# Kernel optimization log

Measured on AMD Instinct MI355X. Metric: run time of the kernel, lower is better.

Reference implementation:

```python
import jax, jax.numpy as jnp
import numpy as np

B, T, C, H, W = 8, 8, 32, 16, 28
NH, DK = 4, 8                 # n_head, d_k == d_v
RADIUS = [3, 3, 3, 3]
DILATION = [1, 3, 5, 7]
LN_EPS = 1e-5


def setup_inputs() -> dict:
    key = jax.random.key(0)
    ks = jax.random.split(key, 8)
    s = 1.0 / np.sqrt(C).astype(np.float32)
    return {
        "first": jax.random.normal(ks[0], (B, T, C, H, W), jnp.float32),
        "x": jax.random.normal(ks[1], (B, T, C, H, W), jnp.float32),
        "Wq": jax.random.normal(ks[2], (NH * DK, C), jnp.float32) * s,
        "Wk": jax.random.normal(ks[3], (NH * DK, C), jnp.float32) * s,
        "Wv": jax.random.normal(ks[4], (NH * DK, C), jnp.float32) * s,
        "Wo": jax.random.normal(ks[5], (C, NH * DK), jnp.float32) * s,
        "ln_gamma": 1.0 + 0.1 * jax.random.normal(ks[6], (DK, H, W), jnp.float32),
        "ln_beta": 0.1 * jax.random.normal(ks[7], (DK, H, W), jnp.float32),
    }


def _shift(x, dy, dx):
    # out[..., i, j] = x[..., i+dy, j+dx]; zero out-of-bounds. mask: (H, W) valid.
    h, w = x.shape[-2:]
    xs = jnp.roll(x, (-dy, -dx), axis=(-2, -1))
    mh = (jnp.arange(h) + dy >= 0) & (jnp.arange(h) + dy < h)
    mw = (jnp.arange(w) + dx >= 0) & (jnp.arange(w) + dx < w)
    m = mh[:, None] & mw[None, :]
    return jnp.where(m, xs, 0.0), m


def _head_attn(q, k, v, radius, dilation, scale):
    # q,k,v: (b,t,c,h,w). Returns softmaxed scores P (b,t,O*t,h,w) and
    # aggregation T (b,t,c,h,w). Aggregation uses RAW scaled scores (as the repo
    # does: spatial_temporal_aggregation receives M_A_i, not its softmax).
    b, t, c, h, w = q.shape
    scores, vals, masks = [], [], []
    for dy in range(-radius, radius + 1):
        for dx in range(-radius, radius + 1):
            ks, m = _shift(k, dy * dilation, dx * dilation)
            vs, _ = _shift(v, dy * dilation, dx * dilation)
            # score against all source frames s at the shifted spatial location
            scores.append(jnp.einsum('btchw,bschw->btshw', q, ks))
            vals.append(vs)
            masks.append(m)
    A = jnp.stack(scores, axis=2)                      # (b,t,O,s,h,w), O=(2r+1)^2
    M = jnp.stack(masks, axis=0)                       # (O,h,w)
    A = jnp.where(M[None, None, :, None], A / scale, -jnp.inf)
    O = A.shape[2]
    P = jax.nn.softmax(A.reshape(b, t, O * t, h, w), axis=2)
    Wm = jnp.where(M[None, None, :, None], A, 0.0)     # skip invalid (-inf) slots
    V = jnp.stack(vals, axis=0)                        # (O,b,s,c,h,w)
    Tout = jnp.einsum('btoshw,obschw->btchw', Wm, V)
    return P, Tout


def reference(first, x, Wq, Wk, Wv, Wo, ln_gamma, ln_beta):
    b, t, c, h, w = x.shape
    q = jnp.einsum('btchw,oc->btohw', first, Wq).reshape(b, t, NH, DK, h, w)
    k = jnp.einsum('btchw,oc->btohw', x, Wk).reshape(b, t, NH, DK, h, w)
    v = jnp.einsum('btchw,oc->btohw', x, Wv).reshape(b, t, NH, DK, h, w)
    scale = float(np.sqrt(C / NH))
    Ps, Ts = [], []
    for i in range(NH):
        qi = q[:, :, i]
        mu = jnp.mean(qi, axis=(2, 3, 4), keepdims=True)
        var = jnp.var(qi, axis=(2, 3, 4), keepdims=True)
        qi = (qi - mu) / jnp.sqrt(var + LN_EPS) * ln_gamma + ln_beta
        P, Ti = _head_attn(qi, k[:, :, i], v[:, :, i], RADIUS[i], DILATION[i], scale)
        Ps.append(P)
        Ts.append(Ti)
    M_S = jnp.max(jnp.concatenate(Ps, axis=2), axis=2)   # (b,t,h,w)
    M_T = jnp.concatenate(Ts, axis=2)                    # (b,t,NH*DK,h,w)
    out = jnp.einsum('btchw,oc->btohw', M_T, Wo) * M_S[:, :, None]
    return out
```

## Files before the change

kernel.cpp:

```cpp
#include <hip/hip_runtime.h>

#define Bc 8
#define Tc 8
#define Cc 32
#define Hc 16
#define Wc 28
#define NHc 4
#define DKc 8
#define HWc (Hc*Wc)
#define INV_SCALE 0.35355339059327373f
#define LN_EPSc 1e-5f

typedef _Float16 half8 __attribute__((ext_vector_type(8)));


__global__ __launch_bounds__(448) void qkv_ln_kernel(
    const float* __restrict__ first, const float* __restrict__ x,
    const float* __restrict__ Wq, const float* __restrict__ Wk,
    const float* __restrict__ Wv,
    const float* __restrict__ gamma, const float* __restrict__ beta,
    float4* __restrict__ Q, float* __restrict__ K, float* __restrict__ V)
{
    int blk  = blockIdx.x;
    int head = blk % NHc;
    int bt   = blk / NHc;
    int t    = bt % Tc;
    int b    = bt / Tc;
    int tid  = threadIdx.x;

    const float* fp = first + (size_t)bt * Cc * HWc + tid;
    const float* xp = x     + (size_t)bt * Cc * HWc + tid;
    float fv[Cc], xv[Cc];
#pragma unroll
    for (int c = 0; c < Cc; ++c) { fv[c] = fp[c*HWc]; xv[c] = xp[c*HWc]; }

    float qv[DKc], kv[DKc], vv[DKc];
#pragma unroll
    for (int dk = 0; dk < DKc; ++dk) {
        int o = head*DKc + dk;
        float aq = 0.f, ak = 0.f, av = 0.f;
#pragma unroll
        for (int c = 0; c < Cc; ++c) {
            aq = fmaf(Wq[o*Cc+c], fv[c], aq);
            ak = fmaf(Wk[o*Cc+c], xv[c], ak);
            av = fmaf(Wv[o*Cc+c], xv[c], av);
        }
        qv[dk] = aq; kv[dk] = ak; vv[dk] = av;
    }

    int bh = b*NHc + head;
    float* kp = K + (((size_t)bh*Tc + t)*HWc + tid)*DKc;
    float* vp = V + (((size_t)bh*Tc + t)*HWc + tid)*DKc;
    *(float4*)(kp)   = make_float4(kv[0],kv[1],kv[2],kv[3]);
    *(float4*)(kp+4) = make_float4(kv[4],kv[5],kv[6],kv[7]);
    *(float4*)(vp)   = make_float4(vv[0],vv[1],vv[2],vv[3]);
    *(float4*)(vp+4) = make_float4(vv[4],vv[5],vv[6],vv[7]);

    float s1 = 0.f, s2 = 0.f;
#pragma unroll
    for (int dk = 0; dk < DKc; ++dk) { s1 += qv[dk]; s2 += qv[dk]*qv[dk]; }
#pragma unroll
    for (int off = 32; off >= 1; off >>= 1) {
        s1 += __shfl_down(s1, off, 64);
        s2 += __shfl_down(s2, off, 64);
    }
    __shared__ float r1[8], r2[8];
    int wid = tid >> 6, lane = tid & 63;
    if (lane == 0) { r1[wid] = s1; r2[wid] = s2; }
    __syncthreads();
    float S1 = 0.f, S2 = 0.f;
#pragma unroll
    for (int wv2 = 0; wv2 < 7; ++wv2) { S1 += r1[wv2]; S2 += r2[wv2]; }
    const float invN = 1.f / (float)(DKc * HWc);
    float mu   = S1 * invN;
    float var  = S2 * invN - mu*mu;
    float rstd = rsqrtf(var + LN_EPSc);

    float qn[DKc];
#pragma unroll
    for (int dk = 0; dk < DKc; ++dk) {
        float gg = gamma[dk*HWc + tid];
        float bb = beta [dk*HWc + tid];
        qn[dk] = ((qv[dk] - mu) * rstd * gg + bb) * INV_SCALE;
    }
    Q[(((size_t)bh*Tc + t)*2 + 0)*HWc + tid] = make_float4(qn[0],qn[1],qn[2],qn[3]);
    Q[(((size_t)bh*Tc + t)*2 + 1)*HWc + tid] = make_float4(qn[4],qn[5],qn[6],qn[7]);
}

__global__ __launch_bounds__(448, 4) void attn_kernel(
    const float4* __restrict__ Q, const float* __restrict__ K,
    const float* __restrict__ V,
    half8* __restrict__ Tpart, float2* __restrict__ LMpart)
{
    int blk  = blockIdx.x;
    int g    = blk & 1;
    int s    = (blk >> 1) & 7;
    int bh   = blk >> 4;
    int head = bh & 3;
    int dil  = 2*head + 1;

    int tid = threadIdx.x;
    int w = tid % Wc;
    int h = tid / Wc;

    __shared__ float4 sK0[HWc], sK1[HWc], sV0[HWc], sV1[HWc];

    const float* kp = K + ((size_t)bh*Tc + s)*HWc*DKc;
    const float* vp = V + ((size_t)bh*Tc + s)*HWc*DKc;
    sK0[tid] = *(const float4*)(kp + tid*DKc);
    sK1[tid] = *(const float4*)(kp + tid*DKc + 4);
    sV0[tid] = *(const float4*)(vp + tid*DKc);
    sV1[tid] = *(const float4*)(vp + tid*DKc + 4);

    const int t0 = g*4;
    float4 q0[4], q1[4];
    const float4* qb = Q + (size_t)bh*Tc*2*HWc + tid;
#pragma unroll
    for (int j = 0; j < 4; ++j) {
        q0[j] = qb[((t0+j)*2+0)*HWc];
        q1[j] = qb[((t0+j)*2+1)*HWc];
    }

    float4 a0[4], a1[4];
    float l[4], m[4];
#pragma unroll
    for (int j = 0; j < 4; ++j) {
        a0[j] = make_float4(0.f,0.f,0.f,0.f);
        a1[j] = make_float4(0.f,0.f,0.f,0.f);
        l[j] = 0.f; m[j] = -1e30f;
    }

    __syncthreads();

    for (int dy = -3; dy <= 3; ++dy) {
        int hy = h + dy*dil;
        if ((unsigned)hy >= (unsigned)Hc) continue;
        int rowbase = hy*Wc;
#pragma unroll
        for (int dx = -3; dx <= 3; ++dx) {
            int wx = w + dx*dil;
            int wcl = min(max(wx, 0), Wc-1);
            bool cv = (unsigned)wx < (unsigned)Wc;
            float bias = cv ? 0.f : -1e30f;
            float mask = cv ? 1.f : 0.f;
            int idx = rowbase + wcl;
            float4 k0 = sK0[idx], k1 = sK1[idx];
            float4 v0 = sV0[idx], v1 = sV1[idx];
#pragma unroll
            for (int j = 0; j < 4; ++j) {
                float sc = q0[j].x*k0.x + q0[j].y*k0.y + q0[j].z*k0.z + q0[j].w*k0.w
                         + q1[j].x*k1.x + q1[j].y*k1.y + q1[j].z*k1.z + q1[j].w*k1.w;
                float msc = sc + bias;
                m[j] = fmaxf(m[j], msc);
                l[j] += __expf(msc);
                float z = sc * mask;
                a0[j].x = fmaf(z, v0.x, a0[j].x);
                a0[j].y = fmaf(z, v0.y, a0[j].y);
                a0[j].z = fmaf(z, v0.z, a0[j].z);
                a0[j].w = fmaf(z, v0.w, a0[j].w);
                a1[j].x = fmaf(z, v1.x, a1[j].x);
                a1[j].y = fmaf(z, v1.y, a1[j].y);
                a1[j].z = fmaf(z, v1.z, a1[j].z);
                a1[j].w = fmaf(z, v1.w, a1[j].w);
            }
        }
    }

    half8*  tp  = Tpart  + (size_t)(bh*Tc + s)*Tc*HWc + tid;
    float2* lmp = LMpart + (size_t)(bh*Tc + s)*Tc*HWc + tid;
#pragma unroll
    for (int j = 0; j < 4; ++j) {
        half8 hv;
        hv[0] = (_Float16)a0[j].x; hv[1] = (_Float16)a0[j].y;
        hv[2] = (_Float16)a0[j].z; hv[3] = (_Float16)a0[j].w;
        hv[4] = (_Float16)a1[j].x; hv[5] = (_Float16)a1[j].y;
        hv[6] = (_Float16)a1[j].z; hv[7] = (_Float16)a1[j].w;
        tp [(t0+j)*HWc] = hv;
        lmp[(t0+j)*HWc] = make_float2(l[j], m[j]);
    }
}

__global__ __launch_bounds__(448) void combine_kernel(
    const half8* __restrict__ Tpart, const float2* __restrict__ LMpart,
    float4* __restrict__ Tout, float* __restrict__ Mprob)
{
    int blk = blockIdx.x;
    int t   = blk & 7;
    int bh  = blk >> 3;
    int tid = threadIdx.x;

    float s0x=0.f,s0y=0.f,s0z=0.f,s0w=0.f;
    float s1x=0.f,s1y=0.f,s1z=0.f,s1w=0.f;
    float lsum = 0.f, mmax = -1e30f;
#pragma unroll
    for (int s = 0; s < Tc; ++s) {
        half8 u = Tpart[(size_t)((bh*Tc + s)*Tc + t)*HWc + tid];
        s0x += (float)u[0]; s0y += (float)u[1]; s0z += (float)u[2]; s0w += (float)u[3];
        s1x += (float)u[4]; s1y += (float)u[5]; s1z += (float)u[6]; s1w += (float)u[7];
        float2 lm = LMpart[(size_t)((bh*Tc + s)*Tc + t)*HWc + tid];
        lsum += lm.x; mmax = fmaxf(mmax, lm.y);
    }
    Tout[(size_t)((bh*Tc + t)*2 + 0)*HWc + tid] = make_float4(s0x,s0y,s0z,s0w);
    Tout[(size_t)((bh*Tc + t)*2 + 1)*HWc + tid] = make_float4(s1x,s1y,s1z,s1w);
    Mprob[(size_t)(bh*Tc + t)*HWc + tid] = __expf(mmax) / lsum;
}

__global__ __launch_bounds__(448) void outproj_kernel(
    const float4* __restrict__ Tout, const float* __restrict__ Mprob,
    const float* __restrict__ Wo, float* __restrict__ out)
{
    int blk = blockIdx.x;
    int og  = blk % 4;
    int bt  = blk / 4;
    int b   = bt / Tc, t = bt % Tc;
    int tid = threadIdx.x;

    float mv[Cc];
    float MS = 0.f;
#pragma unroll
    for (int head = 0; head < NHc; ++head) {
        int bh = b*NHc + head;
        float4 u0 = Tout[(size_t)((bh*Tc + t)*2 + 0)*HWc + tid];
        float4 u1 = Tout[(size_t)((bh*Tc + t)*2 + 1)*HWc + tid];
        mv[head*8+0]=u0.x; mv[head*8+1]=u0.y; mv[head*8+2]=u0.z; mv[head*8+3]=u0.w;
        mv[head*8+4]=u1.x; mv[head*8+5]=u1.y; mv[head*8+6]=u1.z; mv[head*8+7]=u1.w;
        MS = fmaxf(MS, Mprob[(size_t)(bh*Tc + t)*HWc + tid]);
    }
#pragma unroll
    for (int i = 0; i < 8; ++i) {
        int o = og*8 + i;
        float acc = 0.f;
#pragma unroll
        for (int c = 0; c < Cc; ++c) acc = fmaf(Wo[o*Cc+c], mv[c], acc);
        out[((size_t)bt*Cc + o)*HWc + tid] = acc * MS;
    }
}

extern "C" void kernel_launch(void* const* d_in, const int* in_sizes, int n_in,
                              void* d_out, int out_size, void* d_ws, size_t ws_size,
                              hipStream_t stream) {
    const float* first = (const float*)d_in[0];
    const float* x     = (const float*)d_in[1];
    const float* Wq    = (const float*)d_in[2];
    const float* Wk    = (const float*)d_in[3];
    const float* Wv    = (const float*)d_in[4];
    const float* Wo    = (const float*)d_in[5];
    const float* g     = (const float*)d_in[6];
    const float* bta   = (const float*)d_in[7];
    float* out = (float*)d_out;

    float* ws = (float*)d_ws;
    const size_t N5 = (size_t)Bc*NHc*Tc*HWc*DKc;
    float4* Q   = (float4*)ws;
    float*  K   = ws +   N5;
    float*  V   = ws + 2*N5;
    float4* Tt  = (float4*)(ws + 3*N5);
    float*  Mp  = ws + 4*N5;
    half8*  Tp  = (half8*)(ws + 4*N5 + N5/8);
    float2* LMp = (float2*)(ws + 8*N5 + N5/8);

    qkv_ln_kernel <<<Bc*Tc*NHc,   448, 0, stream>>>(first, x, Wq, Wk, Wv, g, bta, Q, K, V);
    attn_kernel   <<<Bc*NHc*Tc*2, 448, 0, stream>>>(Q, K, V, Tp, LMp);
    combine_kernel<<<Bc*NHc*Tc,   448, 0, stream>>>(Tp, LMp, Tt, Mp);
    outproj_kernel<<<Bc*Tc*4,     448, 0, stream>>>(Tt, Mp, Wo, out);
}
```

Before: 137.8 us.

## Pair light and heavy attention heads per block and remap block indices

The attention kernel now processes two heads per block, pairing head ha with head 3-ha so a small-dilation head (many valid neighbors) is balanced against a large-dilation head (many rows skipped). This halves the grid to 256 blocks and evens out per-block work, aiming to reduce tail imbalance across the 256 CUs. The cost is fewer, longer blocks, doubled shared memory per block, and a lower occupancy hint. The qkv and outproj kernels also change their block-index decomposition so consecutive blocks cover different (b,t) rather than different heads or output groups.

```diff
diff --git a/kernel.cpp b/kernel.cpp
--- a/kernel.cpp
+++ b/kernel.cpp
@@ -22,8 +22,8 @@
     float4* __restrict__ Q, float* __restrict__ K, float* __restrict__ V)
 {
     int blk  = blockIdx.x;
-    int head = blk % NHc;
-    int bt   = blk / NHc;
+    int head = blk >> 6;
+    int bt   = blk & 63;
     int t    = bt % Tc;
     int b    = bt / Tc;
     int tid  = threadIdx.x;
@@ -87,32 +87,13 @@
     Q[(((size_t)bh*Tc + t)*2 + 1)*HWc + tid] = make_float4(qn[4],qn[5],qn[6],qn[7]);
 }
 
-__global__ __launch_bounds__(448, 4) void attn_kernel(
-    const float4* __restrict__ Q, const float* __restrict__ K,
-    const float* __restrict__ V,
+__device__ __forceinline__ void attn_item(
+    int bh, int dil, int s, int t0, int tid, int w, int h,
+    const float4* __restrict__ sK0, const float4* __restrict__ sK1,
+    const float4* __restrict__ sV0, const float4* __restrict__ sV1,
+    const float4* __restrict__ Q,
     half8* __restrict__ Tpart, float2* __restrict__ LMpart)
 {
-    int blk  = blockIdx.x;
-    int g    = blk & 1;
-    int s    = (blk >> 1) & 7;
-    int bh   = blk >> 4;
-    int head = bh & 3;
-    int dil  = 2*head + 1;
-
-    int tid = threadIdx.x;
-    int w = tid % Wc;
-    int h = tid / Wc;
-
-    __shared__ float4 sK0[HWc], sK1[HWc], sV0[HWc], sV1[HWc];
-
-    const float* kp = K + ((size_t)bh*Tc + s)*HWc*DKc;
-    const float* vp = V + ((size_t)bh*Tc + s)*HWc*DKc;
-    sK0[tid] = *(const float4*)(kp + tid*DKc);
-    sK1[tid] = *(const float4*)(kp + tid*DKc + 4);
-    sV0[tid] = *(const float4*)(vp + tid*DKc);
-    sV1[tid] = *(const float4*)(vp + tid*DKc + 4);
-
-    const int t0 = g*4;
     float4 q0[4], q1[4];
     const float4* qb = Q + (size_t)bh*Tc*2*HWc + tid;
 #pragma unroll
@@ -129,8 +110,6 @@
         a1[j] = make_float4(0.f,0.f,0.f,0.f);
         l[j] = 0.f; m[j] = -1e30f;
     }
-
-    __syncthreads();
 
     for (int dy = -3; dy <= 3; ++dy) {
         int hy = h + dy*dil;
@@ -180,6 +159,48 @@
     }
 }
 
+__global__ __launch_bounds__(448, 2) void attn_kernel(
+    const float4* __restrict__ Q, const float* __restrict__ K,
+    const float* __restrict__ V,
+    half8* __restrict__ Tpart, float2* __restrict__ LMpart)
+{
+    int blk = blockIdx.x;
+    int g   = blk & 1;
+    int s   = (blk >> 1) & 7;
+    int ha  = (blk >> 4) & 1;
+    int b   = blk >> 5;
+
+    int bhA = b*NHc + ha;            int dilA = 2*ha + 1;
+    int bhB = b*NHc + (3 - ha);      int dilB = 7 - 2*ha;
+
+    int tid = threadIdx.x;
+    int w = tid % Wc;
+    int h = tid / Wc;
+
+    __shared__ float4 sKA0[HWc], sKA1[HWc], sVA0[HWc], sVA1[HWc];
+    __shared__ float4 sKB0[HWc], sKB1[HWc], sVB0[HWc], sVB1[HWc];
+
+    {
+        const float* kpA = K + ((size_t)bhA*Tc + s)*HWc*DKc;
+        const float* vpA = V + ((size_t)bhA*Tc + s)*HWc*DKc;
+        const float* kpB = K + ((size_t)bhB*Tc + s)*HWc*DKc;
+        const float* vpB = V + ((size_t)bhB*Tc + s)*HWc*DKc;
+        sKA0[tid] = *(const float4*)(kpA + tid*DKc);
+        sKA1[tid] = *(const float4*)(kpA + tid*DKc + 4);
+        sVA0[tid] = *(const float4*)(vpA + tid*DKc);
+        sVA1[tid] = *(const float4*)(vpA + tid*DKc + 4);
+        sKB0[tid] = *(const float4*)(kpB + tid*DKc);
+        sKB1[tid] = *(const float4*)(kpB + tid*DKc + 4);
+        sVB0[tid] = *(const float4*)(vpB + tid*DKc);
+        sVB1[tid] = *(const float4*)(vpB + tid*DKc + 4);
+    }
+    __syncthreads();
+
+    int t0 = g*4;
+    attn_item(bhA, dilA, s, t0, tid, w, h, sKA0, sKA1, sVA0, sVA1, Q, Tpart, LMpart);
+    attn_item(bhB, dilB, s, t0, tid, w, h, sKB0, sKB1, sVB0, sVB1, Q, Tpart, LMpart);
+}
+
 __global__ __launch_bounds__(448) void combine_kernel(
     const half8* __restrict__ Tpart, const float2* __restrict__ LMpart,
     float4* __restrict__ Tout, float* __restrict__ Mprob)
@@ -210,8 +231,8 @@
     const float* __restrict__ Wo, float* __restrict__ out)
 {
     int blk = blockIdx.x;
-    int og  = blk % 4;
-    int bt  = blk / 4;
+    int og  = blk >> 6;
+    int bt  = blk & 63;
     int b   = bt / Tc, t = bt % Tc;
     int tid = threadIdx.x;
 
@@ -259,8 +280,8 @@
     half8*  Tp  = (half8*)(ws + 4*N5 + N5/8);
     float2* LMp = (float2*)(ws + 8*N5 + N5/8);
 
-    qkv_ln_kernel <<<Bc*Tc*NHc,   448, 0, stream>>>(first, x, Wq, Wk, Wv, g, bta, Q, K, V);
-    attn_kernel   <<<Bc*NHc*Tc*2, 448, 0, stream>>>(Q, K, V, Tp, LMp);
-    combine_kernel<<<Bc*NHc*Tc,   448, 0, stream>>>(Tp, LMp, Tt, Mp);
-    outproj_kernel<<<Bc*Tc*4,     448, 0, stream>>>(Tt, Mp, Wo, out);
-}
+    qkv_ln_kernel <<<Bc*Tc*NHc, 448, 0, stream>>>(first, x, Wq, Wk, Wv, g, bta, Q, K, V);
+    attn_kernel   <<<256,       448, 0, stream>>>(Q, K, V, Tp, LMp);
+    combine_kernel<<<Bc*NHc*Tc, 448, 0, stream>>>(Tp, LMp, Tt, Mp);
+    outproj_kernel<<<256,       448, 0, stream>>>(Tt, Mp, Wo, out);
+}
```

Result: faster. 123.3 us (-10.6%).

## Fuse combine into output projection and load-balance attention blocks by head dilation

Applied to the files above, without the earlier changes.

Removes the separate combine kernel: the output projection now reduces the per-source-frame partial aggregates and softmax statistics directly, dropping one launch and the intermediate Tout/Mprob round-trip through memory. The attention grid is remapped so the first half of blocks covers the light heads (0,1) and the second half the heavy heads (3,2) in mirrored order, aiming to balance per-head work across the dispatch. The qkv and outproj block index orders are also changed. In exchange, outproj does redundant reduction work: each of its four output-group blocks repeats the same partial-sum reduction.

```diff
diff --git a/kernel.cpp b/kernel.cpp
--- a/kernel.cpp
+++ b/kernel.cpp
@@ -22,8 +22,8 @@
     float4* __restrict__ Q, float* __restrict__ K, float* __restrict__ V)
 {
     int blk  = blockIdx.x;
-    int head = blk % NHc;
-    int bt   = blk / NHc;
+    int head = blk >> 6;
+    int bt   = blk & 63;
     int t    = bt % Tc;
     int b    = bt / Tc;
     int tid  = threadIdx.x;
@@ -92,12 +92,18 @@
     const float* __restrict__ V,
     half8* __restrict__ Tpart, float2* __restrict__ LMpart)
 {
-    int blk  = blockIdx.x;
-    int g    = blk & 1;
-    int s    = (blk >> 1) & 7;
-    int bh   = blk >> 4;
-    int head = bh & 3;
+    int blk = blockIdx.x;
+    int p   = blk >> 8;
+    int i   = blk & 255;
+    int b   = i >> 5;
+    int ha  = (i >> 4) & 1;
+    int s   = (i >> 1) & 7;
+    int th  = i & 1;
+
+    int head = p ? (3 - ha) : ha;
     int dil  = 2*head + 1;
+    int bh   = b*NHc + head;
+    int t0   = th*4;
 
     int tid = threadIdx.x;
     int w = tid % Wc;
@@ -112,7 +118,6 @@
     sV0[tid] = *(const float4*)(vp + tid*DKc);
     sV1[tid] = *(const float4*)(vp + tid*DKc + 4);
 
-    const int t0 = g*4;
     float4 q0[4], q1[4];
     const float4* qb = Q + (size_t)bh*Tc*2*HWc + tid;
 #pragma unroll
@@ -180,39 +185,14 @@
     }
 }
 
-__global__ __launch_bounds__(448) void combine_kernel(
+__global__ __launch_bounds__(448) void outproj_kernel(
     const half8* __restrict__ Tpart, const float2* __restrict__ LMpart,
-    float4* __restrict__ Tout, float* __restrict__ Mprob)
-{
-    int blk = blockIdx.x;
-    int t   = blk & 7;
-    int bh  = blk >> 3;
-    int tid = threadIdx.x;
-
-    float s0x=0.f,s0y=0.f,s0z=0.f,s0w=0.f;
-    float s1x=0.f,s1y=0.f,s1z=0.f,s1w=0.f;
-    float lsum = 0.f, mmax = -1e30f;
-#pragma unroll
-    for (int s = 0; s < Tc; ++s) {
-        half8 u = Tpart[(size_t)((bh*Tc + s)*Tc + t)*HWc + tid];
-        s0x += (float)u[0]; s0y += (float)u[1]; s0z += (float)u[2]; s0w += (float)u[3];
-        s1x += (float)u[4]; s1y += (float)u[5]; s1z += (float)u[6]; s1w += (float)u[7];
-        float2 lm = LMpart[(size_t)((bh*Tc + s)*Tc + t)*HWc + tid];
-        lsum += lm.x; mmax = fmaxf(mmax, lm.y);
-    }
-    Tout[(size_t)((bh*Tc + t)*2 + 0)*HWc + tid] = make_float4(s0x,s0y,s0z,s0w);
-    Tout[(size_t)((bh*Tc + t)*2 + 1)*HWc + tid] = make_float4(s1x,s1y,s1z,s1w);
-    Mprob[(size_t)(bh*Tc + t)*HWc + tid] = __expf(mmax) / lsum;
-}
-
-__global__ __launch_bounds__(448) void outproj_kernel(
-    const float4* __restrict__ Tout, const float* __restrict__ Mprob,
     const float* __restrict__ Wo, float* __restrict__ out)
 {
     int blk = blockIdx.x;
-    int og  = blk % 4;
-    int bt  = blk / 4;
-    int b   = bt / Tc, t = bt % Tc;
+    int og  = blk >> 6;
+    int bt  = blk & 63;
+    int b   = bt >> 3, t = bt & 7;
     int tid = threadIdx.x;
 
     float mv[Cc];
@@ -220,19 +200,29 @@
 #pragma unroll
     for (int head = 0; head < NHc; ++head) {
         int bh = b*NHc + head;
-        float4 u0 = Tout[(size_t)((bh*Tc + t)*2 + 0)*HWc + tid];
-        float4 u1 = Tout[(size_t)((bh*Tc + t)*2 + 1)*HWc + tid];
-        mv[head*8+0]=u0.x; mv[head*8+1]=u0.y; mv[head*8+2]=u0.z; mv[head*8+3]=u0.w;
-        mv[head*8+4]=u1.x; mv[head*8+5]=u1.y; mv[head*8+6]=u1.z; mv[head*8+7]=u1.w;
-        MS = fmaxf(MS, Mprob[(size_t)(bh*Tc + t)*HWc + tid]);
+        float acc[DKc];
+#pragma unroll
+        for (int j = 0; j < DKc; ++j) acc[j] = 0.f;
+        float lsum = 0.f, mmax = -1e30f;
+#pragma unroll
+        for (int s = 0; s < Tc; ++s) {
+            half8 u = Tpart[(size_t)((bh*Tc + s)*Tc + t)*HWc + tid];
+#pragma unroll
+            for (int j = 0; j < DKc; ++j) acc[j] += (float)u[j];
+            float2 lm = LMpart[(size_t)((bh*Tc + s)*Tc + t)*HWc + tid];
+            lsum += lm.x; mmax = fmaxf(mmax, lm.y);
+        }
+#pragma unroll
+        for (int j = 0; j < DKc; ++j) mv[head*DKc + j] = acc[j];
+        MS = fmaxf(MS, __expf(mmax) / lsum);
     }
 #pragma unroll
     for (int i = 0; i < 8; ++i) {
         int o = og*8 + i;
-        float acc = 0.f;
-#pragma unroll
-        for (int c = 0; c < Cc; ++c) acc = fmaf(Wo[o*Cc+c], mv[c], acc);
-        out[((size_t)bt*Cc + o)*HWc + tid] = acc * MS;
+        float a = 0.f;
+#pragma unroll
+        for (int c = 0; c < Cc; ++c) a = fmaf(Wo[o*Cc+c], mv[c], a);
+        out[((size_t)bt*Cc + o)*HWc + tid] = a * MS;
     }
 }
 
@@ -254,13 +244,10 @@
     float4* Q   = (float4*)ws;
     float*  K   = ws +   N5;
     float*  V   = ws + 2*N5;
-    float4* Tt  = (float4*)(ws + 3*N5);
-    float*  Mp  = ws + 4*N5;
-    half8*  Tp  = (half8*)(ws + 4*N5 + N5/8);
-    float2* LMp = (float2*)(ws + 8*N5 + N5/8);
-
-    qkv_ln_kernel <<<Bc*Tc*NHc,   448, 0, stream>>>(first, x, Wq, Wk, Wv, g, bta, Q, K, V);
-    attn_kernel   <<<Bc*NHc*Tc*2, 448, 0, stream>>>(Q, K, V, Tp, LMp);
-    combine_kernel<<<Bc*NHc*Tc,   448, 0, stream>>>(Tp, LMp, Tt, Mp);
-    outproj_kernel<<<Bc*Tc*4,     448, 0, stream>>>(Tt, Mp, Wo, out);
-}
+    half8*  Tp  = (half8*)(ws + 3*N5);
+    float2* LMp = (float2*)(ws + 7*N5);
+
+    qkv_ln_kernel <<<Bc*Tc*NHc, 448, 0, stream>>>(first, x, Wq, Wk, Wv, g, bta, Q, K, V);
+    attn_kernel   <<<512,       448, 0, stream>>>(Q, K, V, Tp, LMp);
+    outproj_kernel<<<256,       448, 0, stream>>>(Tp, LMp, Wo, out);
+}
```

Measured after the change: 127.4 us. 7.6% less time.
